# Performance work log

Measured on AMD Instinct MI355X. Metric: run time of the kernel, lower is better.

## Reference

```python
import jax, jax.numpy as jnp
import numpy as np

N_NODES = 100000
N_EDGES = 1600000
IN_CH = 128
HID = 128
EPS = 1e-5


def setup_inputs() -> dict:
    key = jax.random.key(0)
    ks = jax.random.split(key, 16)
    x = jax.random.normal(ks[0], (N_NODES, IN_CH), dtype=jnp.float32)
    edge_index = jax.random.randint(ks[1], (2, N_EDGES), 0, N_NODES, dtype=jnp.int64)
    dims = [(IN_CH, HID), (HID, HID), (HID, HID // 2)]
    params = {}
    for i, (di, do) in enumerate(dims):
        params[f'w{i}'] = jax.random.normal(ks[2 + i], (di, do), dtype=jnp.float32) * (1.0 / np.sqrt(di))
        params[f'b{i}'] = jnp.zeros((do,), dtype=jnp.float32)
        params[f'g{i}'] = jnp.ones((do,), dtype=jnp.float32)
        params[f'be{i}'] = jnp.zeros((do,), dtype=jnp.float32)
    params['wc1'] = jax.random.normal(ks[8], (HID // 2, 32), dtype=jnp.float32) * (1.0 / np.sqrt(HID // 2))
    params['bc1'] = jnp.zeros((32,), dtype=jnp.float32)
    params['wc2'] = jax.random.normal(ks[9], (32, 1), dtype=jnp.float32) * (1.0 / np.sqrt(32))
    params['bc2'] = jnp.zeros((1,), dtype=jnp.float32)
    return {'x': x, 'edge_index': edge_index, **params}


def _gcn_forward(x, edge_index, w0, b0, g0, be0, w1, b1, g1, be1, w2, b2, g2, be2, wc1, bc1, wc2, bc2):
    n = x.shape[0]
    # add self-loops (GCNConv default)
    loops = jnp.arange(n, dtype=edge_index.dtype)
    src = jnp.concatenate([edge_index[0], loops])  # [E+N]
    dst = jnp.concatenate([edge_index[1], loops])
    # symmetric normalization: deg over targets (incl. self loops)
    deg = jax.ops.segment_sum(jnp.ones_like(dst, dtype=x.dtype), dst, num_segments=n)
    dis = jax.lax.rsqrt(jnp.maximum(deg, 1e-12))  # deg>=1 due to self loops
    norm = (dis[src] * dis[dst])[:, None]  # [E+N, 1]

    def layer(h, w, b, g, be):
        h = h @ w                                   # [N, d_out]
        h = jax.ops.segment_sum(h[src] * norm, dst, num_segments=n) + b
        mu = jnp.mean(h, axis=0)
        var = jnp.mean(jnp.square(h - mu), axis=0)  # biased var (torch BN)
        h = (h - mu) * jax.lax.rsqrt(var + EPS) * g + be
        return jax.nn.relu(h)                       # dropout: identity (eval)

    h = layer(x, w0, b0, g0, be0)
    h = layer(h, w1, b1, g1, be1)
    h = layer(h, w2, b2, g2, be2)
    h = jax.nn.relu(h @ wc1 + bc1)
    return (h @ wc2 + bc2)[:, 0]  # [N]


def reference(x, edge_index, w0, b0, g0, be0, w1, b1, g1, be1, w2, b2, g2, be2, wc1, bc1, wc2, bc2):
    return _gcn_forward(x, edge_index, w0, b0, g0, be0, w1, b1, g1, be1, w2, b2, g2, be2, wc1, bc1, wc2, bc2)
```

## Files before the change

kernel.cpp:

```cpp
#include <hip/hip_runtime.h>


typedef __attribute__((ext_vector_type(8))) short short8;
typedef __attribute__((ext_vector_type(4))) float f32x4;

#define BIN_SHIFT 7
#define BIN_NODES 128
#define CAPB 4096
#define CAP 64
#define SPARTS 1024

__device__ __forceinline__ float b2f(unsigned short u) {
    return __uint_as_float(((unsigned)u) << 16);
}
__device__ __forceinline__ unsigned short f2bf(float f) {
    unsigned u = __float_as_uint(f);
    return (unsigned short)((u + 0x7fff + ((u >> 16) & 1)) >> 16);
}

__global__ __launch_bounds__(256) void part1_kernel(const int* __restrict__ eidx,
                                                    int E, int nbins, int chunk,
                                                    int* __restrict__ bin_fill,
                                                    int* __restrict__ binned) {
    __shared__ int cntS[1024];
    __shared__ int baseS[1024];
    int tid = threadIdx.x;
    for (int b = tid; b < nbins; b += 256) cntS[b] = 0;
    __syncthreads();
    int e0 = blockIdx.x * chunk;
    int e1 = min(e0 + chunk, E);
    for (int e = e0 + tid; e < e1; e += 256)
        atomicAdd(&cntS[eidx[E + e] >> BIN_SHIFT], 1);
    __syncthreads();
    for (int b = tid; b < nbins; b += 256) {
        baseS[b] = atomicAdd(&bin_fill[b], cntS[b]);
        cntS[b] = 0;
    }
    __syncthreads();
    for (int e = e0 + tid; e < e1; e += 256) {
        int d = eidx[E + e];
        int s = eidx[e];
        int b = d >> BIN_SHIFT;
        int p = baseS[b] + atomicAdd(&cntS[b], 1);
        if (p < CAPB) binned[b * CAPB + p] = (s << BIN_SHIFT) | (d & (BIN_NODES - 1));
    }
}

__global__ __launch_bounds__(256) void part2_kernel(const int* __restrict__ bin_fill,
                                                    const int* __restrict__ binned,
                                                    int N, int* __restrict__ fill,
                                                    float* __restrict__ dis,
                                                    int* __restrict__ stage) {
    __shared__ int lfill[BIN_NODES];
    int b = blockIdx.x, tid = threadIdx.x;
    if (tid < BIN_NODES) lfill[tid] = 0;
    __syncthreads();
    int cnt = min(bin_fill[b], CAPB);
    const int* seg = binned + b * CAPB;
    for (int i = tid; i < cnt; i += 256) {
        int v = seg[i];
        int dl = v & (BIN_NODES - 1);
        int p = atomicAdd(&lfill[dl], 1);
        int node = (b << BIN_SHIFT) + dl;
        if (p < CAP) stage[(node << 6) + p] = v >> BIN_SHIFT;
    }
    __syncthreads();
    if (tid < BIN_NODES) {
        int node = (b << BIN_SHIFT) + tid;
        if (node < N) {
            int c = lfill[tid];
            fill[node] = c;
            dis[node] = rsqrtf((float)c + 1.0f);
        }
    }
}

__global__ void wfrag_kernel(const float* __restrict__ w0,
                             const float* __restrict__ w1,
                             const float* __restrict__ w2,
                             unsigned short* __restrict__ wf) {
    int tid = blockIdx.x * 256 + threadIdx.x;
    if (tid >= 40960) return;
    const float* w;
    int idx, C;
    if (tid < 16384) { w = w0; idx = tid; C = 128; }
    else if (tid < 32768) { w = w1; idx = tid - 16384; C = 128; }
    else { w = w2; idx = tid - 32768; C = 64; }
    int j = idx & 7;
    int lane = (idx >> 3) & 63;
    int q = (idx >> 9) & 3;
    int n_tile = idx >> 11;
    int k = q * 32 + (lane >> 4) * 8 + j;
    int n = n_tile * 16 + (lane & 15);
    wf[tid] = f2bf(w[k * C + n]);
}

__device__ __forceinline__ void load8(const float* p, float4& lo, float4& hi) {
    lo = *(const float4*)p;
    hi = *(const float4*)(p + 4);
}
__device__ __forceinline__ void load8(const unsigned short* p, float4& lo, float4& hi) {
    int4 q = *(const int4*)p;
    lo = make_float4(__uint_as_float((unsigned)q.x << 16),
                     __uint_as_float((unsigned)q.x & 0xffff0000u),
                     __uint_as_float((unsigned)q.y << 16),
                     __uint_as_float((unsigned)q.y & 0xffff0000u));
    hi = make_float4(__uint_as_float((unsigned)q.z << 16),
                     __uint_as_float((unsigned)q.z & 0xffff0000u),
                     __uint_as_float((unsigned)q.w << 16),
                     __uint_as_float((unsigned)q.w & 0xffff0000u));
}

template <int C, typename InT>
__global__ __launch_bounds__(256, 5) void mfma_gemm_kernel(
    const InT* __restrict__ xin, const unsigned short* __restrict__ wf,
    const float* __restrict__ scale, const float* __restrict__ shift,
    const float* __restrict__ dis, unsigned short* __restrict__ out, int N) {
    constexpr int NT = C / 16;
    constexpr int WFRAGS = NT * 4 * 64;
    __shared__ short8 ws[WFRAGS];
    int tid = threadIdx.x;
    for (int i = tid; i < WFRAGS; i += 256) ws[i] = ((const short8*)wf)[i];

    int lane = tid & 63;
    int wave = tid >> 6;
    int m0 = blockIdx.x * 64 + wave * 16;
    int r15 = lane & 15, r4 = lane >> 4;
    f32x4 acc[NT];
#pragma unroll
    for (int t = 0; t < NT; t++) acc[t] = (f32x4){0.f, 0.f, 0.f, 0.f};
    int row0 = m0 + r15;
    int row0c = min(row0, N - 1);
    __syncthreads();

#pragma unroll
    for (int q = 0; q < 4; q++) {
        int kb = q * 32 + r4 * 8;
        float4 a0l, a0h;
        load8(xin + (size_t)row0c * 128 + kb, a0l, a0h);
        if (scale) {
            float4 scl = *(const float4*)&scale[kb];
            float4 sch = *(const float4*)&scale[kb + 4];
            float4 shl = *(const float4*)&shift[kb];
            float4 shh = *(const float4*)&shift[kb + 4];
            a0l.x = fmaxf(a0l.x * scl.x + shl.x, 0.f);
            a0l.y = fmaxf(a0l.y * scl.y + shl.y, 0.f);
            a0l.z = fmaxf(a0l.z * scl.z + shl.z, 0.f);
            a0l.w = fmaxf(a0l.w * scl.w + shl.w, 0.f);
            a0h.x = fmaxf(a0h.x * sch.x + shh.x, 0.f);
            a0h.y = fmaxf(a0h.y * sch.y + shh.y, 0.f);
            a0h.z = fmaxf(a0h.z * sch.z + shh.z, 0.f);
            a0h.w = fmaxf(a0h.w * sch.w + shh.w, 0.f);
        }
        short8 a0;
        a0[0] = (short)f2bf(a0l.x); a0[1] = (short)f2bf(a0l.y);
        a0[2] = (short)f2bf(a0l.z); a0[3] = (short)f2bf(a0l.w);
        a0[4] = (short)f2bf(a0h.x); a0[5] = (short)f2bf(a0h.y);
        a0[6] = (short)f2bf(a0h.z); a0[7] = (short)f2bf(a0h.w);
#pragma unroll
        for (int nt = 0; nt < NT; nt++) {
            short8 b = ws[(nt * 4 + q) * 64 + lane];
            acc[nt] = __builtin_amdgcn_mfma_f32_16x16x32_bf16(a0, b, acc[nt], 0, 0, 0);
        }
    }
    float d0r[4];
#pragma unroll
    for (int r = 0; r < 4; r++) {
        int rowa = m0 + r4 * 4 + r;
        d0r[r] = (rowa < N) ? dis[rowa] : 0.f;
    }
#pragma unroll
    for (int nt = 0; nt < NT; nt++) {
        int col = nt * 16 + r15;
#pragma unroll
        for (int r = 0; r < 4; r++) {
            int rowa = m0 + r4 * 4 + r;
            if (rowa < N) out[(size_t)rowa * C + col] = f2bf(acc[nt][r] * d0r[r]);
        }
    }
}

__global__ __launch_bounds__(256) void agg128_kernel(
    const unsigned short* __restrict__ h, const int* __restrict__ fill,
    const int* __restrict__ stage, const float* __restrict__ dis,
    unsigned short* __restrict__ out, int N) {
    int lane = threadIdx.x & 63;
    int node = blockIdx.x * 4 + (threadIdx.x >> 6);
    if (node >= N) return;
    float dn = dis[node];
    ushort2 sv = ((const ushort2*)(h + (size_t)node * 128))[lane];
    float2 acc = make_float2(b2f(sv.x), b2f(sv.y));
    int ne = min(fill[node], CAP);
    int pk = (lane < ne) ? stage[(node << 6) + lane] : 0;
    int j = 0;
    for (; j + 16 <= ne; j += 16) {
        ushort2 a[16];
#pragma unroll
        for (int t = 0; t < 16; t++) {
            int s = __builtin_amdgcn_readlane(pk, j + t);
            a[t] = ((const ushort2*)(h + (size_t)s * 128))[lane];
        }
#pragma unroll
        for (int t = 0; t < 16; t++) { acc.x += b2f(a[t].x); acc.y += b2f(a[t].y); }
    }
    for (; j + 8 <= ne; j += 8) {
        ushort2 a[8];
#pragma unroll
        for (int t = 0; t < 8; t++) {
            int s = __builtin_amdgcn_readlane(pk, j + t);
            a[t] = ((const ushort2*)(h + (size_t)s * 128))[lane];
        }
#pragma unroll
        for (int t = 0; t < 8; t++) { acc.x += b2f(a[t].x); acc.y += b2f(a[t].y); }
    }
    for (; j + 4 <= ne; j += 4) {
        ushort2 a[4];
#pragma unroll
        for (int t = 0; t < 4; t++) {
            int s = __builtin_amdgcn_readlane(pk, j + t);
            a[t] = ((const ushort2*)(h + (size_t)s * 128))[lane];
        }
#pragma unroll
        for (int t = 0; t < 4; t++) { acc.x += b2f(a[t].x); acc.y += b2f(a[t].y); }
    }
    for (; j < ne; j++) {
        int s = __builtin_amdgcn_readlane(pk, j);
        ushort2 a = ((const ushort2*)(h + (size_t)s * 128))[lane];
        acc.x += b2f(a.x);
        acc.y += b2f(a.y);
    }
    ((ushort2*)(out + (size_t)node * 128))[lane] =
        make_ushort2(f2bf(acc.x * dn), f2bf(acc.y * dn));
}

__global__ __launch_bounds__(256) void agg64_kernel(
    const unsigned short* __restrict__ h, const int* __restrict__ fill,
    const int* __restrict__ stage, const float* __restrict__ dis,
    unsigned short* __restrict__ out, int N) {
    int lane = threadIdx.x & 63;
    int node = blockIdx.x * 4 + (threadIdx.x >> 6);
    if (node >= N) return;
    int half = lane >> 5, ch = lane & 31;
    float dn = dis[node];
    float2 acc = make_float2(0.f, 0.f);
    if (half == 0) {
        ushort2 sv = ((const ushort2*)(h + (size_t)node * 64))[ch];
        acc.x = b2f(sv.x);
        acc.y = b2f(sv.y);
    }
    int ne = min(fill[node], CAP);
    int pk = (lane < ne) ? stage[(node << 6) + lane] : 0;
    int j = 0;
    for (; j + 16 <= ne; j += 16) {
        ushort2 a[8];
#pragma unroll
        for (int t = 0; t < 8; t++) {
            int s = __shfl(pk, j + 2 * t + half);
            a[t] = ((const ushort2*)(h + (size_t)s * 64))[ch];
        }
#pragma unroll
        for (int t = 0; t < 8; t++) { acc.x += b2f(a[t].x); acc.y += b2f(a[t].y); }
    }
    for (; j + 8 <= ne; j += 8) {
        ushort2 a[4];
#pragma unroll
        for (int t = 0; t < 4; t++) {
            int s = __shfl(pk, j + 2 * t + half);
            a[t] = ((const ushort2*)(h + (size_t)s * 64))[ch];
        }
#pragma unroll
        for (int t = 0; t < 4; t++) { acc.x += b2f(a[t].x); acc.y += b2f(a[t].y); }
    }
    for (; j < ne; j += 2) {
        int jj = j + half;
        int s = __shfl(pk, jj);
        bool v = jj < ne;
        ushort2 a = ((const ushort2*)(h + (size_t)s * 64))[ch];
        acc.x += v ? b2f(a.x) : 0.f;
        acc.y += v ? b2f(a.y) : 0.f;
    }
    acc.x += __shfl_down(acc.x, 32);
    acc.y += __shfl_down(acc.y, 32);
    if (half == 0)
        ((ushort2*)(out + (size_t)node * 64))[ch] =
            make_ushort2(f2bf(acc.x * dn), f2bf(acc.y * dn));
}

template <int C>
__global__ __launch_bounds__(256) void stats1_kernel(const unsigned short* __restrict__ h,
                                                     int N, float* __restrict__ partials) {
    constexpr int CG = C / 4;
    constexpr int RG = 256 / CG;
    int t = threadIdx.x;
    int cg = t % CG;
    int rg = t / CG;
    float s[4] = {0.f, 0.f, 0.f, 0.f}, q[4] = {0.f, 0.f, 0.f, 0.f};
    for (int n = blockIdx.x * RG + rg; n < N; n += gridDim.x * RG) {
        ushort4 v = *(const ushort4*)&h[(size_t)n * C + cg * 4];
        float f0 = b2f(v.x), f1 = b2f(v.y), f2 = b2f(v.z), f3 = b2f(v.w);
        s[0] += f0; s[1] += f1; s[2] += f2; s[3] += f3;
        q[0] += f0 * f0; q[1] += f1 * f1; q[2] += f2 * f2; q[3] += f3 * f3;
    }
    __shared__ float red[256 * 8];
#pragma unroll
    for (int k = 0; k < 4; k++) {
        red[(rg * CG + cg) * 8 + k] = s[k];
        red[(rg * CG + cg) * 8 + 4 + k] = q[k];
    }
    __syncthreads();
    if (rg == 0) {
#pragma unroll
        for (int w = 1; w < RG; w++)
#pragma unroll
            for (int k = 0; k < 4; k++) {
                s[k] += red[(w * CG + cg) * 8 + k];
                q[k] += red[(w * CG + cg) * 8 + 4 + k];
            }
        float* pb = partials + (size_t)blockIdx.x * 2 * C;
#pragma unroll
        for (int k = 0; k < 4; k++) {
            pb[cg * 4 + k] = s[k];
            pb[C + cg * 4 + k] = q[k];
        }
    }
}

template <int C>
__global__ __launch_bounds__(256) void stats2_kernel(const float* __restrict__ partials,
                                                     const float* __restrict__ g,
                                                     const float* __restrict__ be, int N,
                                                     float* __restrict__ scale,
                                                     float* __restrict__ shift) {
    int c = blockIdx.x;
    int t = threadIdx.x;
    float s = 0.f, q = 0.f;
    for (int b = t; b < SPARTS; b += 256) {
        const float* pb = partials + (size_t)b * 2 * C;
        s += pb[c];
        q += pb[C + c];
    }
    __shared__ float rs[256], rq[256];
    rs[t] = s;
    rq[t] = q;
    __syncthreads();
    for (int d = 128; d > 0; d >>= 1) {
        if (t < d) {
            rs[t] += rs[t + d];
            rq[t] += rq[t + d];
        }
        __syncthreads();
    }
    if (t == 0) {
        float inv_n = 1.0f / (float)N;
        float mean = rs[0] * inv_n;
        float var = rq[0] * inv_n - mean * mean;
        var = var > 0.f ? var : 0.f;
        float sc = g[c] * rsqrtf(var + 1e-5f);
        scale[c] = sc;
        shift[c] = be[c] - mean * sc;
    }
}

__global__ __launch_bounds__(256) void head_kernel(
    const unsigned short* __restrict__ h, const float* __restrict__ scale,
    const float* __restrict__ shift, const float* __restrict__ wc1,
    const float* __restrict__ bc1, const float* __restrict__ wc2,
    const float* __restrict__ bc2, float* __restrict__ out, int N) {
    __shared__ float w1s[64 * 32];
    __shared__ float b1s[32], w2s[32], s2s[64], sh2[64];
    __shared__ float b2s;
    int tid = threadIdx.x;
    for (int i = tid; i < 64 * 32; i += 256) w1s[i] = wc1[i];
    if (tid < 32) { b1s[tid] = bc1[tid]; w2s[tid] = wc2[tid]; }
    if (tid < 64) { s2s[tid] = scale[tid]; sh2[tid] = shift[tid]; }
    if (tid == 0) b2s = bc2[0];
    __syncthreads();
    int n = blockIdx.x * 256 + tid;
    if (n >= N) return;
    float v[64];
#pragma unroll
    for (int k = 0; k < 64; k++) {
        float x = b2f(h[(size_t)n * 64 + k]) * s2s[k] + sh2[k];
        v[k] = x > 0.f ? x : 0.f;
    }
    float o = b2s;
#pragma unroll 2
    for (int j = 0; j < 32; j++) {
        float t = b1s[j];
#pragma unroll
        for (int k = 0; k < 64; k++) t += v[k] * w1s[k * 32 + j];
        t = t > 0.f ? t : 0.f;
        o += t * w2s[j];
    }
    out[n] = o;
}

extern "C" void kernel_launch(void* const* d_in, const int* in_sizes, int n_in,
                              void* d_out, int out_size, void* d_ws, size_t ws_size,
                              hipStream_t stream) {
    const float* x = (const float*)d_in[0];
    const int* eidx = (const int*)d_in[1];
    const float* w0 = (const float*)d_in[2];
    const float* g0 = (const float*)d_in[4];
    const float* be0 = (const float*)d_in[5];
    const float* w1 = (const float*)d_in[6];
    const float* g1 = (const float*)d_in[8];
    const float* be1 = (const float*)d_in[9];
    const float* w2 = (const float*)d_in[10];
    const float* g2 = (const float*)d_in[12];
    const float* be2 = (const float*)d_in[13];
    const float* wc1 = (const float*)d_in[14];
    const float* bc1 = (const float*)d_in[15];
    const float* wc2 = (const float*)d_in[16];
    const float* bc2 = (const float*)d_in[17];

    const int N = in_sizes[0] / 128;
    const int E = in_sizes[1] / 2;
    const int nbins = (N + BIN_NODES - 1) >> BIN_SHIFT;

    char* p = (char*)d_ws;
    auto alloc = [&](size_t bytes) {
        void* r = (void*)p;
        p += (bytes + 255) & ~(size_t)255;
        return r;
    };
    int* bin_fill = (int*)alloc((size_t)nbins * 4);
    size_t zero_bytes = (size_t)(p - (char*)d_ws);
    int* fill = (int*)alloc((size_t)N * 4);
    int* binned = (int*)alloc((size_t)nbins * CAPB * 4);
    int* stage = (int*)alloc((size_t)N * CAP * 4);
    float* dis = (float*)alloc((size_t)N * 4);
    float* ss = (float*)alloc(3 * 256 * 4);
    float* partials = (float*)alloc((size_t)SPARTS * 256 * 4);
    unsigned short* hA = (unsigned short*)alloc((size_t)N * 128 * 2);
    unsigned short* hB = (unsigned short*)alloc((size_t)N * 128 * 2);
    unsigned short* wf = (unsigned short*)alloc(40960 * 2);
    unsigned short* wf0 = wf;
    unsigned short* wf1 = wf + 16384;
    unsigned short* wf2 = wf + 32768;

    float* sc0 = ss, *sh0 = ss + 128;
    float* sc1 = ss + 256, *sh1 = ss + 384;
    float* sc2 = ss + 512, *sh2 = ss + 640;

    hipMemsetAsync(d_ws, 0, zero_bytes, stream);

    wfrag_kernel<<<160, 256, 0, stream>>>(w0, w1, w2, wf);
    int p1_blocks = 256;
    int chunk = (E + p1_blocks - 1) / p1_blocks;
    part1_kernel<<<p1_blocks, 256, 0, stream>>>(eidx, E, nbins, chunk, bin_fill, binned);
    part2_kernel<<<nbins, 256, 0, stream>>>(bin_fill, binned, N, fill, dis, stage);

    int agg_grid = (N + 3) / 4;
    int gemm_grid = (N + 63) / 64;

    mfma_gemm_kernel<128, float><<<gemm_grid, 256, 0, stream>>>(x, wf0, nullptr, nullptr,
                                                                dis, hA, N);
    agg128_kernel<<<agg_grid, 256, 0, stream>>>(hA, fill, stage, dis, hB, N);
    stats1_kernel<128><<<SPARTS, 256, 0, stream>>>(hB, N, partials);
    stats2_kernel<128><<<128, 256, 0, stream>>>(partials, g0, be0, N, sc0, sh0);

    mfma_gemm_kernel<128, unsigned short><<<gemm_grid, 256, 0, stream>>>(
        hB, wf1, sc0, sh0, dis, hA, N);
    agg128_kernel<<<agg_grid, 256, 0, stream>>>(hA, fill, stage, dis, hB, N);
    stats1_kernel<128><<<SPARTS, 256, 0, stream>>>(hB, N, partials);
    stats2_kernel<128><<<128, 256, 0, stream>>>(partials, g1, be1, N, sc1, sh1);

    mfma_gemm_kernel<64, unsigned short><<<gemm_grid, 256, 0, stream>>>(
        hB, wf2, sc1, sh1, dis, hA, N);
    agg64_kernel<<<agg_grid, 256, 0, stream>>>(hA, fill, stage, dis, hB, N);
    stats1_kernel<64><<<SPARTS, 256, 0, stream>>>(hB, N, partials);
    stats2_kernel<64><<<64, 256, 0, stream>>>(partials, g2, be2, N, sc2, sh2);

    head_kernel<<<(N + 255) / 256, 256, 0, stream>>>(hB, sc2, sh2, wc1, bc1, wc2,
                                                     bc2, (float*)d_out, N);
}
```

Before: 435.5 us.

## Replace atomic bin allocation with count/scan/place passes and fold weight prep

```diff
diff --git a/kernel.cpp b/kernel.cpp
--- a/kernel.cpp
+++ b/kernel.cpp
@@ -9,6 +9,7 @@
 #define CAPB 4096
 #define CAP 64
 #define SPARTS 1024
+#define P1B 256
 
 __device__ __forceinline__ float b2f(unsigned short u) {
     return __uint_as_float(((unsigned)u) << 16);
@@ -18,25 +19,70 @@
     return (unsigned short)((u + 0x7fff + ((u >> 16) & 1)) >> 16);
 }
 
-__global__ __launch_bounds__(256) void part1_kernel(const int* __restrict__ eidx,
-                                                    int E, int nbins, int chunk,
-                                                    int* __restrict__ bin_fill,
-                                                    int* __restrict__ binned) {
+__global__ __launch_bounds__(256) void count_kernel(
+    const int* __restrict__ eidx, int E, int nbins, int chunk,
+    int* __restrict__ cntG,
+    const float* __restrict__ w0, const float* __restrict__ w1,
+    const float* __restrict__ w2, unsigned short* __restrict__ wf) {
     __shared__ int cntS[1024];
-    __shared__ int baseS[1024];
     int tid = threadIdx.x;
-    for (int b = tid; b < nbins; b += 256) cntS[b] = 0;
+    for (int b = tid; b < 1024; b += 256) cntS[b] = 0;
+
+    int tg = blockIdx.x * 256 + tid;
+    if (tg < 40960) {
+        const float* w;
+        int idx, C;
+        if (tg < 16384) { w = w0; idx = tg; C = 128; }
+        else if (tg < 32768) { w = w1; idx = tg - 16384; C = 128; }
+        else { w = w2; idx = tg - 32768; C = 64; }
+        int j = idx & 7;
+        int lane = (idx >> 3) & 63;
+        int q = (idx >> 9) & 3;
+        int n_tile = idx >> 11;
+        int k = q * 32 + (lane >> 4) * 8 + j;
+        int n = n_tile * 16 + (lane & 15);
+        wf[tg] = f2bf(w[k * C + n]);
+    }
     __syncthreads();
     int e0 = blockIdx.x * chunk;
     int e1 = min(e0 + chunk, E);
     for (int e = e0 + tid; e < e1; e += 256)
         atomicAdd(&cntS[eidx[E + e] >> BIN_SHIFT], 1);
     __syncthreads();
+    for (int b = tid; b < nbins; b += 256)
+        cntG[b * P1B + blockIdx.x] = cntS[b];
+}
+
+__global__ __launch_bounds__(P1B) void scan_kernel(int* __restrict__ cntG,
+                                                   int* __restrict__ bin_fill) {
+    __shared__ int sh[P1B];
+    int b = blockIdx.x, t = threadIdx.x;
+    int v = cntG[b * P1B + t];
+    sh[t] = v;
+    __syncthreads();
+    for (int d = 1; d < P1B; d <<= 1) {
+        int u = (t >= d) ? sh[t - d] : 0;
+        __syncthreads();
+        sh[t] += u;
+        __syncthreads();
+    }
+    cntG[b * P1B + t] = sh[t] - v;
+    if (t == P1B - 1) bin_fill[b] = sh[P1B - 1];
+}
+
+__global__ __launch_bounds__(256) void place_kernel(
+    const int* __restrict__ eidx, int E, int nbins, int chunk,
+    const int* __restrict__ baseG, int* __restrict__ binned) {
+    __shared__ int cntS[1024];
+    __shared__ int baseS[1024];
+    int tid = threadIdx.x;
     for (int b = tid; b < nbins; b += 256) {
-        baseS[b] = atomicAdd(&bin_fill[b], cntS[b]);
+        baseS[b] = baseG[b * P1B + blockIdx.x];
         cntS[b] = 0;
     }
     __syncthreads();
+    int e0 = blockIdx.x * chunk;
+    int e1 = min(e0 + chunk, E);
     for (int e = e0 + tid; e < e1; e += 256) {
         int d = eidx[E + e];
         int s = eidx[e];
@@ -73,26 +119,6 @@
             dis[node] = rsqrtf((float)c + 1.0f);
         }
     }
-}
-
-__global__ void wfrag_kernel(const float* __restrict__ w0,
-                             const float* __restrict__ w1,
-                             const float* __restrict__ w2,
-                             unsigned short* __restrict__ wf) {
-    int tid = blockIdx.x * 256 + threadIdx.x;
-    if (tid >= 40960) return;
-    const float* w;
-    int idx, C;
-    if (tid < 16384) { w = w0; idx = tid; C = 128; }
-    else if (tid < 32768) { w = w1; idx = tid - 16384; C = 128; }
-    else { w = w2; idx = tid - 32768; C = 64; }
-    int j = idx & 7;
-    int lane = (idx >> 3) & 63;
-    int q = (idx >> 9) & 3;
-    int n_tile = idx >> 11;
-    int k = q * 32 + (lane >> 4) * 8 + j;
-    int n = n_tile * 16 + (lane & 15);
-    wf[tid] = f2bf(w[k * C + n]);
 }
 
 __device__ __forceinline__ void load8(const float* p, float4& lo, float4& hi) {
@@ -425,7 +451,6 @@
         return r;
     };
     int* bin_fill = (int*)alloc((size_t)nbins * 4);
-    size_t zero_bytes = (size_t)(p - (char*)d_ws);
     int* fill = (int*)alloc((size_t)N * 4);
     int* binned = (int*)alloc((size_t)nbins * CAPB * 4);
     int* stage = (int*)alloc((size_t)N * CAP * 4);
@@ -443,12 +468,12 @@
     float* sc1 = ss + 256, *sh1 = ss + 384;
     float* sc2 = ss + 512, *sh2 = ss + 640;
 
-    hipMemsetAsync(d_ws, 0, zero_bytes, stream);
-
-    wfrag_kernel<<<160, 256, 0, stream>>>(w0, w1, w2, wf);
-    int p1_blocks = 256;
-    int chunk = (E + p1_blocks - 1) / p1_blocks;
-    part1_kernel<<<p1_blocks, 256, 0, stream>>>(eidx, E, nbins, chunk, bin_fill, binned);
+    int* cntG = (int*)partials;
+
+    int chunk = (E + P1B - 1) / P1B;
+    count_kernel<<<P1B, 256, 0, stream>>>(eidx, E, nbins, chunk, cntG, w0, w1, w2, wf);
+    scan_kernel<<<nbins, P1B, 0, stream>>>(cntG, bin_fill);
+    place_kernel<<<P1B, 256, 0, stream>>>(eidx, E, nbins, chunk, cntG, binned);
     part2_kernel<<<nbins, 256, 0, stream>>>(bin_fill, binned, N, fill, dis, stage);
 
     int agg_grid = (N + 3) / 4;
```

New measurement: 436.2 us. About the same (+0.2%).

## Fuse BN stats into aggregation, replace binned CSR build with direct atomic scatter

Applied to the files above, without the earlier changes.

```diff
diff --git a/kernel.cpp b/kernel.cpp
--- a/kernel.cpp
+++ b/kernel.cpp
@@ -4,11 +4,8 @@
 typedef __attribute__((ext_vector_type(8))) short short8;
 typedef __attribute__((ext_vector_type(4))) float f32x4;
 
-#define BIN_SHIFT 7
-#define BIN_NODES 128
-#define CAPB 4096
 #define CAP 64
-#define SPARTS 1024
+#define AGB 2048
 
 __device__ __forceinline__ float b2f(unsigned short u) {
     return __uint_as_float(((unsigned)u) << 16);
@@ -18,81 +15,32 @@
     return (unsigned short)((u + 0x7fff + ((u >> 16) & 1)) >> 16);
 }
 
-__global__ __launch_bounds__(256) void part1_kernel(const int* __restrict__ eidx,
-                                                    int E, int nbins, int chunk,
-                                                    int* __restrict__ bin_fill,
-                                                    int* __restrict__ binned) {
-    __shared__ int cntS[1024];
-    __shared__ int baseS[1024];
-    int tid = threadIdx.x;
-    for (int b = tid; b < nbins; b += 256) cntS[b] = 0;
-    __syncthreads();
-    int e0 = blockIdx.x * chunk;
-    int e1 = min(e0 + chunk, E);
-    for (int e = e0 + tid; e < e1; e += 256)
-        atomicAdd(&cntS[eidx[E + e] >> BIN_SHIFT], 1);
-    __syncthreads();
-    for (int b = tid; b < nbins; b += 256) {
-        baseS[b] = atomicAdd(&bin_fill[b], cntS[b]);
-        cntS[b] = 0;
-    }
-    __syncthreads();
-    for (int e = e0 + tid; e < e1; e += 256) {
+__global__ __launch_bounds__(256) void scatter_kernel(
+    const int* __restrict__ eidx, int E, int N, int* __restrict__ fill,
+    int* __restrict__ stage, const float* __restrict__ w0,
+    const float* __restrict__ w1, const float* __restrict__ w2,
+    unsigned short* __restrict__ wf) {
+    int tg = blockIdx.x * 256 + threadIdx.x;
+    if (tg < 40960) {
+        const float* w;
+        int idx, C;
+        if (tg < 16384) { w = w0; idx = tg; C = 128; }
+        else if (tg < 32768) { w = w1; idx = tg - 16384; C = 128; }
+        else { w = w2; idx = tg - 32768; C = 64; }
+        int j = idx & 7;
+        int lane = (idx >> 3) & 63;
+        int q = (idx >> 9) & 3;
+        int n_tile = idx >> 11;
+        int k = q * 32 + (lane >> 4) * 8 + j;
+        int n = n_tile * 16 + (lane & 15);
+        wf[tg] = f2bf(w[k * C + n]);
+    }
+    for (int e = tg; e < E; e += gridDim.x * 256) {
+        int s = eidx[e];
         int d = eidx[E + e];
-        int s = eidx[e];
-        int b = d >> BIN_SHIFT;
-        int p = baseS[b] + atomicAdd(&cntS[b], 1);
-        if (p < CAPB) binned[b * CAPB + p] = (s << BIN_SHIFT) | (d & (BIN_NODES - 1));
-    }
-}
-
-__global__ __launch_bounds__(256) void part2_kernel(const int* __restrict__ bin_fill,
-                                                    const int* __restrict__ binned,
-                                                    int N, int* __restrict__ fill,
-                                                    float* __restrict__ dis,
-                                                    int* __restrict__ stage) {
-    __shared__ int lfill[BIN_NODES];
-    int b = blockIdx.x, tid = threadIdx.x;
-    if (tid < BIN_NODES) lfill[tid] = 0;
-    __syncthreads();
-    int cnt = min(bin_fill[b], CAPB);
-    const int* seg = binned + b * CAPB;
-    for (int i = tid; i < cnt; i += 256) {
-        int v = seg[i];
-        int dl = v & (BIN_NODES - 1);
-        int p = atomicAdd(&lfill[dl], 1);
-        int node = (b << BIN_SHIFT) + dl;
-        if (p < CAP) stage[(node << 6) + p] = v >> BIN_SHIFT;
-    }
-    __syncthreads();
-    if (tid < BIN_NODES) {
-        int node = (b << BIN_SHIFT) + tid;
-        if (node < N) {
-            int c = lfill[tid];
-            fill[node] = c;
-            dis[node] = rsqrtf((float)c + 1.0f);
-        }
-    }
-}
-
-__global__ void wfrag_kernel(const float* __restrict__ w0,
-                             const float* __restrict__ w1,
-                             const float* __restrict__ w2,
-                             unsigned short* __restrict__ wf) {
-    int tid = blockIdx.x * 256 + threadIdx.x;
-    if (tid >= 40960) return;
-    const float* w;
-    int idx, C;
-    if (tid < 16384) { w = w0; idx = tid; C = 128; }
-    else if (tid < 32768) { w = w1; idx = tid - 16384; C = 128; }
-    else { w = w2; idx = tid - 32768; C = 64; }
-    int j = idx & 7;
-    int lane = (idx >> 3) & 63;
-    int q = (idx >> 9) & 3;
-    int n_tile = idx >> 11;
-    int k = q * 32 + (lane >> 4) * 8 + j;
-    int n = n_tile * 16 + (lane & 15);
-    wf[tid] = f2bf(w[k * C + n]);
+        int p = atomicAdd(&fill[d], 1);
+        if (p < CAP) stage[(d << 6) + p] = s;
+    }
 }
 
 __device__ __forceinline__ void load8(const float* p, float4& lo, float4& hi) {
@@ -115,7 +63,7 @@
 __global__ __launch_bounds__(256, 5) void mfma_gemm_kernel(
     const InT* __restrict__ xin, const unsigned short* __restrict__ wf,
     const float* __restrict__ scale, const float* __restrict__ shift,
-    const float* __restrict__ dis, unsigned short* __restrict__ out, int N) {
+    const int* __restrict__ fill, unsigned short* __restrict__ out, int N) {
     constexpr int NT = C / 16;
     constexpr int WFRAGS = NT * 4 * 64;
     __shared__ short8 ws[WFRAGS];
@@ -129,8 +77,7 @@
     f32x4 acc[NT];
 #pragma unroll
     for (int t = 0; t < NT; t++) acc[t] = (f32x4){0.f, 0.f, 0.f, 0.f};
-    int row0 = m0 + r15;
-    int row0c = min(row0, N - 1);
+    int row0c = min(m0 + r15, N - 1);
     __syncthreads();
 
 #pragma unroll
@@ -167,7 +114,7 @@
 #pragma unroll
     for (int r = 0; r < 4; r++) {
         int rowa = m0 + r4 * 4 + r;
-        d0r[r] = (rowa < N) ? dis[rowa] : 0.f;
+        d0r[r] = (rowa < N) ? rsqrtf((float)fill[rowa] + 1.0f) : 0.f;
     }
 #pragma unroll
     for (int nt = 0; nt < NT; nt++) {
@@ -180,161 +127,164 @@
     }
 }
 
-__global__ __launch_bounds__(256) void agg128_kernel(
+__global__ __launch_bounds__(256) void agg128s_kernel(
     const unsigned short* __restrict__ h, const int* __restrict__ fill,
-    const int* __restrict__ stage, const float* __restrict__ dis,
-    unsigned short* __restrict__ out, int N) {
+    const int* __restrict__ stage, unsigned short* __restrict__ out,
+    float* __restrict__ partials, int N) {
     int lane = threadIdx.x & 63;
-    int node = blockIdx.x * 4 + (threadIdx.x >> 6);
-    if (node >= N) return;
-    float dn = dis[node];
-    ushort2 sv = ((const ushort2*)(h + (size_t)node * 128))[lane];
-    float2 acc = make_float2(b2f(sv.x), b2f(sv.y));
-    int ne = min(fill[node], CAP);
-    int pk = (lane < ne) ? stage[(node << 6) + lane] : 0;
-    int j = 0;
-    for (; j + 16 <= ne; j += 16) {
-        ushort2 a[16];
-#pragma unroll
-        for (int t = 0; t < 16; t++) {
-            int s = __builtin_amdgcn_readlane(pk, j + t);
-            a[t] = ((const ushort2*)(h + (size_t)s * 128))[lane];
-        }
-#pragma unroll
-        for (int t = 0; t < 16; t++) { acc.x += b2f(a[t].x); acc.y += b2f(a[t].y); }
-    }
-    for (; j + 8 <= ne; j += 8) {
-        ushort2 a[8];
-#pragma unroll
-        for (int t = 0; t < 8; t++) {
-            int s = __builtin_amdgcn_readlane(pk, j + t);
-            a[t] = ((const ushort2*)(h + (size_t)s * 128))[lane];
-        }
-#pragma unroll
-        for (int t = 0; t < 8; t++) { acc.x += b2f(a[t].x); acc.y += b2f(a[t].y); }
-    }
-    for (; j + 4 <= ne; j += 4) {
-        ushort2 a[4];
-#pragma unroll
-        for (int t = 0; t < 4; t++) {
-            int s = __builtin_amdgcn_readlane(pk, j + t);
-            a[t] = ((const ushort2*)(h + (size_t)s * 128))[lane];
-        }
-#pragma unroll
-        for (int t = 0; t < 4; t++) { acc.x += b2f(a[t].x); acc.y += b2f(a[t].y); }
-    }
-    for (; j < ne; j++) {
-        int s = __builtin_amdgcn_readlane(pk, j);
-        ushort2 a = ((const ushort2*)(h + (size_t)s * 128))[lane];
-        acc.x += b2f(a.x);
-        acc.y += b2f(a.y);
-    }
-    ((ushort2*)(out + (size_t)node * 128))[lane] =
-        make_ushort2(f2bf(acc.x * dn), f2bf(acc.y * dn));
-}
-
-__global__ __launch_bounds__(256) void agg64_kernel(
+    int wave = threadIdx.x >> 6;
+    int ngroups = (N + 3) >> 2;
+    float2 s = make_float2(0.f, 0.f), qq = make_float2(0.f, 0.f);
+    for (int g = blockIdx.x; g < ngroups; g += gridDim.x) {
+        int node = g * 4 + wave;
+        bool valid = node < N;
+        int nodec = valid ? node : 0;
+        float dn = rsqrtf((float)fill[nodec] + 1.0f);
+        ushort2 sv = ((const ushort2*)(h + (size_t)nodec * 128))[lane];
+        float2 acc = make_float2(b2f(sv.x), b2f(sv.y));
+        int ne = valid ? min(fill[nodec], CAP) : 0;
+        int pk = (lane < ne) ? stage[(nodec << 6) + lane] : 0;
+        int j = 0;
+        for (; j + 16 <= ne; j += 16) {
+            ushort2 a[16];
+#pragma unroll
+            for (int t = 0; t < 16; t++) {
+                int src = __builtin_amdgcn_readlane(pk, j + t);
+                a[t] = ((const ushort2*)(h + (size_t)src * 128))[lane];
+            }
+#pragma unroll
+            for (int t = 0; t < 16; t++) { acc.x += b2f(a[t].x); acc.y += b2f(a[t].y); }
+        }
+        for (; j + 8 <= ne; j += 8) {
+            ushort2 a[8];
+#pragma unroll
+            for (int t = 0; t < 8; t++) {
+                int src = __builtin_amdgcn_readlane(pk, j + t);
+                a[t] = ((const ushort2*)(h + (size_t)src * 128))[lane];
+            }
+#pragma unroll
+            for (int t = 0; t < 8; t++) { acc.x += b2f(a[t].x); acc.y += b2f(a[t].y); }
+        }
+        for (; j + 4 <= ne; j += 4) {
+            ushort2 a[4];
+#pragma unroll
+            for (int t = 0; t < 4; t++) {
+                int src = __builtin_amdgcn_readlane(pk, j + t);
+                a[t] = ((const ushort2*)(h + (size_t)src * 128))[lane];
+            }
+#pragma unroll
+            for (int t = 0; t < 4; t++) { acc.x += b2f(a[t].x); acc.y += b2f(a[t].y); }
+        }
+        for (; j < ne; j++) {
+            int src = __builtin_amdgcn_readlane(pk, j);
+            ushort2 a = ((const ushort2*)(h + (size_t)src * 128))[lane];
+            acc.x += b2f(a.x);
+            acc.y += b2f(a.y);
+        }
+        if (valid) {
+            unsigned short rx = f2bf(acc.x * dn), ry = f2bf(acc.y * dn);
+            ((ushort2*)(out + (size_t)node * 128))[lane] = make_ushort2(rx, ry);
+            float fx = b2f(rx), fy = b2f(ry);
+            s.x += fx; s.y += fy;
+            qq.x += fx * fx; qq.y += fy * fy;
+        }
+    }
+    __shared__ float red[4][256];
+    red[wave][2 * lane] = s.x;
+    red[wave][2 * lane + 1] = s.y;
+    red[wave][128 + 2 * lane] = qq.x;
+    red[wave][128 + 2 * lane + 1] = qq.y;
+    __syncthreads();
+    int t = threadIdx.x;
+    partials[(size_t)blockIdx.x * 256 + t] =
+        red[0][t] + red[1][t] + red[2][t] + red[3][t];
+}
+
+__global__ __launch_bounds__(256) void agg64s_kernel(
     const unsigned short* __restrict__ h, const int* __restrict__ fill,
-    const int* __restrict__ stage, const float* __restrict__ dis,
-    unsigned short* __restrict__ out, int N) {
+    const int* __restrict__ stage, unsigned short* __restrict__ out,
+    float* __restrict__ partials, int N) {
     int lane = threadIdx.x & 63;
-    int node = blockIdx.x * 4 + (threadIdx.x >> 6);
-    if (node >= N) return;
+    int wave = threadIdx.x >> 6;
     int half = lane >> 5, ch = lane & 31;
-    float dn = dis[node];
-    float2 acc = make_float2(0.f, 0.f);
+    int ngroups = (N + 3) >> 2;
+    float2 s = make_float2(0.f, 0.f), qq = make_float2(0.f, 0.f);
+    for (int g = blockIdx.x; g < ngroups; g += gridDim.x) {
+        int node = g * 4 + wave;
+        bool valid = node < N;
+        int nodec = valid ? node : 0;
+        float dn = rsqrtf((float)fill[nodec] + 1.0f);
+        float2 acc = make_float2(0.f, 0.f);
+        if (half == 0) {
+            ushort2 sv = ((const ushort2*)(h + (size_t)nodec * 64))[ch];
+            acc.x = b2f(sv.x);
+            acc.y = b2f(sv.y);
+        }
+        int ne = valid ? min(fill[nodec], CAP) : 0;
+        int pk = (lane < ne) ? stage[(nodec << 6) + lane] : 0;
+        int j = 0;
+        for (; j + 16 <= ne; j += 16) {
+            ushort2 a[8];
+#pragma unroll
+            for (int t = 0; t < 8; t++) {
+                int src = __shfl(pk, j + 2 * t + half);
+                a[t] = ((const ushort2*)(h + (size_t)src * 64))[ch];
+            }
+#pragma unroll
+            for (int t = 0; t < 8; t++) { acc.x += b2f(a[t].x); acc.y += b2f(a[t].y); }
+        }
+        for (; j + 8 <= ne; j += 8) {
+            ushort2 a[4];
+#pragma unroll
+            for (int t = 0; t < 4; t++) {
+                int src = __shfl(pk, j + 2 * t + half);
+                a[t] = ((const ushort2*)(h + (size_t)src * 64))[ch];
+            }
+#pragma unroll
+            for (int t = 0; t < 4; t++) { acc.x += b2f(a[t].x); acc.y += b2f(a[t].y); }
+        }
+        for (; j < ne; j += 2) {
+            int jj = j + half;
+            int src = __shfl(pk, jj);
+            bool v = jj < ne;
+            ushort2 a = ((const ushort2*)(h + (size_t)src * 64))[ch];
+            acc.x += v ? b2f(a.x) : 0.f;
+            acc.y += v ? b2f(a.y) : 0.f;
+        }
+        acc.x += __shfl_down(acc.x, 32);
+        acc.y += __shfl_down(acc.y, 32);
+        if (valid && half == 0) {
+            unsigned short rx = f2bf(acc.x * dn), ry = f2bf(acc.y * dn);
+            ((ushort2*)(out + (size_t)node * 64))[ch] = make_ushort2(rx, ry);
+            float fx = b2f(rx), fy = b2f(ry);
+            s.x += fx; s.y += fy;
+            qq.x += fx * fx; qq.y += fy * fy;
+        }
+    }
+    __shared__ float red[4][128];
     if (half == 0) {
-        ushort2 sv = ((const ushort2*)(h + (size_t)node * 64))[ch];
-        acc.x = b2f(sv.x);
-        acc.y = b2f(sv.y);
-    }
-    int ne = min(fill[node], CAP);
-    int pk = (lane < ne) ? stage[(node << 6) + lane] : 0;
-    int j = 0;
-    for (; j + 16 <= ne; j += 16) {
-        ushort2 a[8];
-#pragma unroll
-        for (int t = 0; t < 8; t++) {
-            int s = __shfl(pk, j + 2 * t + half);
-            a[t] = ((const ushort2*)(h + (size_t)s * 64))[ch];
-        }
-#pragma unroll
-        for (int t = 0; t < 8; t++) { acc.x += b2f(a[t].x); acc.y += b2f(a[t].y); }
-    }
-    for (; j + 8 <= ne; j += 8) {
-        ushort2 a[4];
-#pragma unroll
-        for (int t = 0; t < 4; t++) {
-            int s = __shfl(pk, j + 2 * t + half);
-            a[t] = ((const ushort2*)(h + (size_t)s * 64))[ch];
-        }
-#pragma unroll
-        for (int t = 0; t < 4; t++) { acc.x += b2f(a[t].x); acc.y += b2f(a[t].y); }
-    }
-    for (; j < ne; j += 2) {
-        int jj = j + half;
-        int s = __shfl(pk, jj);
-        bool v = jj < ne;
-        ushort2 a = ((const ushort2*)(h + (size_t)s * 64))[ch];
-        acc.x += v ? b2f(a.x) : 0.f;
-        acc.y += v ? b2f(a.y) : 0.f;
-    }
-    acc.x += __shfl_down(acc.x, 32);
-    acc.y += __shfl_down(acc.y, 32);
-    if (half == 0)
-        ((ushort2*)(out + (size_t)node * 64))[ch] =
-            make_ushort2(f2bf(acc.x * dn), f2bf(acc.y * dn));
-}
-
-template <int C>
-__global__ __launch_bounds__(256) void stats1_kernel(const unsigned short* __restrict__ h,
-                                                     int N, float* __restrict__ partials) {
-    constexpr int CG = C / 4;
-    constexpr int RG = 256 / CG;
+        red[wave][2 * ch] = s.x;
+        red[wave][2 * ch + 1] = s.y;
+        red[wave][64 + 2 * ch] = qq.x;
+        red[wave][64 + 2 * ch + 1] = qq.y;
+    }
+    __syncthreads();
     int t = threadIdx.x;
-    int cg = t % CG;
-    int rg = t / CG;
-    float s[4] = {0.f, 0.f, 0.f, 0.f}, q[4] = {0.f, 0.f, 0.f, 0.f};
-    for (int n = blockIdx.x * RG + rg; n < N; n += gridDim.x * RG) {
-        ushort4 v = *(const ushort4*)&h[(size_t)n * C + cg * 4];
-        float f0 = b2f(v.x), f1 = b2f(v.y), f2 = b2f(v.z), f3 = b2f(v.w);
-        s[0] += f0; s[1] += f1; s[2] += f2; s[3] += f3;
-        q[0] += f0 * f0; q[1] += f1 * f1; q[2] += f2 * f2; q[3] += f3 * f3;
-    }
-    __shared__ float red[256 * 8];
-#pragma unroll
-    for (int k = 0; k < 4; k++) {
-        red[(rg * CG + cg) * 8 + k] = s[k];
-        red[(rg * CG + cg) * 8 + 4 + k] = q[k];
-    }
-    __syncthreads();
-    if (rg == 0) {
-#pragma unroll
-        for (int w = 1; w < RG; w++)
-#pragma unroll
-            for (int k = 0; k < 4; k++) {
-                s[k] += red[(w * CG + cg) * 8 + k];
-                q[k] += red[(w * CG + cg) * 8 + 4 + k];
-            }
-        float* pb = partials + (size_t)blockIdx.x * 2 * C;
-#pragma unroll
-        for (int k = 0; k < 4; k++) {
-            pb[cg * 4 + k] = s[k];
-            pb[C + cg * 4 + k] = q[k];
-        }
-    }
+    if (t < 128)
+        partials[(size_t)blockIdx.x * 128 + t] =
+            red[0][t] + red[1][t] + red[2][t] + red[3][t];
 }
 
 template <int C>
 __global__ __launch_bounds__(256) void stats2_kernel(const float* __restrict__ partials,
                                                      const float* __restrict__ g,
                                                      const float* __restrict__ be, int N,
-                                                     float* __restrict__ scale,
+                                                     int nparts, float* __restrict__ scale,
                                                      float* __restrict__ shift) {
     int c = blockIdx.x;
     int t = threadIdx.x;
     float s = 0.f, q = 0.f;
-    for (int b = t; b < SPARTS; b += 256) {
+    for (int b = t; b < nparts; b += 256) {
         const float* pb = partials + (size_t)b * 2 * C;
         s += pb[c];
         q += pb[C + c];
@@ -416,7 +366,6 @@
 
     const int N = in_sizes[0] / 128;
     const int E = in_sizes[1] / 2;
-    const int nbins = (N + BIN_NODES - 1) >> BIN_SHIFT;
 
     char* p = (char*)d_ws;
     auto alloc = [&](size_t bytes) {
@@ -424,14 +373,10 @@
         p += (bytes + 255) & ~(size_t)255;
         return r;
     };
-    int* bin_fill = (int*)alloc((size_t)nbins * 4);
-    size_t zero_bytes = (size_t)(p - (char*)d_ws);
     int* fill = (int*)alloc((size_t)N * 4);
-    int* binned = (int*)alloc((size_t)nbins * CAPB * 4);
     int* stage = (int*)alloc((size_t)N * CAP * 4);
-    float* dis = (float*)alloc((size_t)N * 4);
     float* ss = (float*)alloc(3 * 256 * 4);
-    float* partials = (float*)alloc((size_t)SPARTS * 256 * 4);
+    float* partials = (float*)alloc((size_t)AGB * 256 * 4);
     unsigned short* hA = (unsigned short*)alloc((size_t)N * 128 * 2);
     unsigned short* hB = (unsigned short*)alloc((size_t)N * 128 * 2);
     unsigned short* wf = (unsigned short*)alloc(40960 * 2);
@@ -443,34 +388,26 @@
     float* sc1 = ss + 256, *sh1 = ss + 384;
     float* sc2 = ss + 512, *sh2 = ss + 640;
 
-    hipMemsetAsync(d_ws, 0, zero_bytes, stream);
-
-    wfrag_kernel<<<160, 256, 0, stream>>>(w0, w1, w2, wf);
-    int p1_blocks = 256;
-    int chunk = (E + p1_blocks - 1) / p1_blocks;
-    part1_kernel<<<p1_blocks, 256, 0, stream>>>(eidx, E, nbins, chunk, bin_fill, binned);
-    part2_kernel<<<nbins, 256, 0, stream>>>(bin_fill, binned, N, fill, dis, stage);
-
-    int agg_grid = (N + 3) / 4;
+    hipMemsetAsync(fill, 0, (size_t)N * 4, stream);
+
+    scatter_kernel<<<1024, 256, 0, stream>>>(eidx, E, N, fill, stage, w0, w1, w2, wf);
+
     int gemm_grid = (N + 63) / 64;
 
     mfma_gemm_kernel<128, float><<<gemm_grid, 256, 0, stream>>>(x, wf0, nullptr, nullptr,
-                                                                dis, hA, N);
-    agg128_kernel<<<agg_grid, 256, 0, stream>>>(hA, fill, stage, dis, hB, N);
-    stats1_kernel<128><<<SPARTS, 256, 0, stream>>>(hB, N, partials);
-    stats2_kernel<128><<<128, 256, 0, stream>>>(partials, g0, be0, N, sc0, sh0);
+                                                                fill, hA, N);
+    agg128s_kernel<<<AGB, 256, 0, stream>>>(hA, fill, stage, hB, partials, N);
+    stats2_kernel<128><<<128, 256, 0, stream>>>(partials, g0, be0, N, AGB, sc0, sh0);
 
     mfma_gemm_kernel<128, unsigned short><<<gemm_grid, 256, 0, stream>>>(
-        hB, wf1, sc0, sh0, dis, hA, N);
-    agg128_kernel<<<agg_grid, 256, 0, stream>>>(hA, fill, stage, dis, hB, N);
-    stats1_kernel<128><<<SPARTS, 256, 0, stream>>>(hB, N, partials);
-    stats2_kernel<128><<<128, 256, 0, stream>>>(partials, g1, be1, N, sc1, sh1);
+        hB, wf1, sc0, sh0, fill, hA, N);
+    agg128s_kernel<<<AGB, 256, 0, stream>>>(hA, fill, stage, hB, partials, N);
+    stats2_kernel<128><<<128, 256, 0, stream>>>(partials, g1, be1, N, AGB, sc1, sh1);
 
     mfma_gemm_kernel<64, unsigned short><<<gemm_grid, 256, 0, stream>>>(
-        hB, wf2, sc1, sh1, dis, hA, N);
-    agg64_kernel<<<agg_grid, 256, 0, stream>>>(hA, fill, stage, dis, hB, N);
-    stats1_kernel<64><<<SPARTS, 256, 0, stream>>>(hB, N, partials);
-    stats2_kernel<64><<<64, 256, 0, stream>>>(partials, g2, be2, N, sc2, sh2);
+        hB, wf2, sc1, sh1, fill, hA, N);
+    agg64s_kernel<<<AGB, 256, 0, stream>>>(hA, fill, stage, hB, partials, N);
+    stats2_kernel<64><<<64, 256, 0, stream>>>(partials, g2, be2, N, AGB, sc2, sh2);
 
     head_kernel<<<(N + 255) / 256, 256, 0, stream>>>(hB, sc2, sh2, wc1, bc1, wc2,
                                                      bc2, (float*)d_out, N);
```

After: 501.1 us. 1.15x slower.
